# Optimization experiments

Hardware: AMD Instinct MI355X
Metric: run time of the kernel (lower is better)

## Reference

```python
import jax, jax.numpy as jnp
import numpy as np

B, F, E, K, O = 4096, 64, 16, 8, 32
NFEAT, HID = 100000, 1024
EPS = 1e-5
N_ITER = 50  # entmax bisection iterations (entmax package default)


def entmax15(x):
    # alpha=1.5 entmax via bisection, faithful to EntmaxBisectFunction.forward
    d = x.shape[-1]
    xs = x * 0.5  # X * (alpha - 1)
    mx = jnp.max(xs, axis=-1, keepdims=True)
    tau_lo = mx - 1.0                      # gp(1, 1.5) = 1
    tau_hi = mx - (1.0 / d) ** 0.5         # gp(1/d, 1.5)
    f_lo = jnp.sum(jnp.square(jnp.maximum(xs - tau_lo, 0.0)), -1, keepdims=True) - 1.0
    dm = tau_hi - tau_lo

    def body(i, carry):
        tau_lo, dm, _ = carry
        dm = dm * 0.5
        tau_m = tau_lo + dm
        f_m = jnp.sum(jnp.square(jnp.maximum(xs - tau_m, 0.0)), -1, keepdims=True) - 1.0
        tau_lo = jnp.where(f_m * f_lo >= 0, tau_m, tau_lo)
        return (tau_lo, dm, tau_m)

    _, _, tau_m = jax.lax.fori_loop(0, N_ITER, body, (tau_lo, dm, tau_lo))
    p = jnp.square(jnp.maximum(xs - tau_m, 0.0))
    return p / jnp.sum(p, -1, keepdims=True)


def bn_channels(x, g, b):
    # BatchNorm1d on (B, C, L): normalize over batch and L per channel C (train mode)
    m = jnp.mean(x, (0, 2), keepdims=True)
    v = jnp.var(x, (0, 2), keepdims=True)
    return (x - m) / jnp.sqrt(v + EPS) * g[None, :, None] + b[None, :, None]


def bn_feat(x, g, b):
    # BatchNorm1d on (B, C) (train mode, biased variance)
    m = jnp.mean(x, 0)
    v = jnp.var(x, 0)
    return (x - m) / jnp.sqrt(v + EPS) * g + b


def setup_inputs() -> dict:
    key = jax.random.key(0)
    ks = jax.random.split(key, 12)
    gain = 1.414
    aQ = gain * np.sqrt(6.0 / (O + E))
    aB = gain * np.sqrt(6.0 / (E + E))
    aV = gain * np.sqrt(6.0 / (O + F))
    D0 = K * O * E
    return {
        'x_id': jax.random.randint(ks[0], (B, F), 0, NFEAT),
        'x_value': jax.random.uniform(ks[1], (B, F), dtype=jnp.float32),
        'emb': jax.random.normal(ks[2], (NFEAT, E), dtype=jnp.float32) * 0.1,
        'emb_g': jnp.ones((F,), jnp.float32), 'emb_b': jnp.zeros((F,), jnp.float32),
        'Q': jax.random.uniform(ks[3], (K, O, E), jnp.float32, -aQ, aQ),
        'bil': jax.random.uniform(ks[4], (K, E, E), jnp.float32, -aB, aB),
        'vals': jax.random.uniform(ks[5], (K, O, F), jnp.float32, -aV, aV),
        'arm_g': jnp.ones((K * O,), jnp.float32), 'arm_b': jnp.zeros((K * O,), jnp.float32),
        'w1': jax.random.normal(ks[6], (HID, D0), jnp.float32) / np.sqrt(D0),
        'b1': jnp.zeros((HID,), jnp.float32),
        'g1': jnp.ones((HID,), jnp.float32), 'bt1': jnp.zeros((HID,), jnp.float32),
        'w2': jax.random.normal(ks[7], (HID, HID), jnp.float32) / np.sqrt(HID),
        'b2': jnp.zeros((HID,), jnp.float32),
        'g2': jnp.ones((HID,), jnp.float32), 'bt2': jnp.zeros((HID,), jnp.float32),
        'wout': jax.random.normal(ks[8], (1, HID), jnp.float32) / np.sqrt(HID),
        'bout': jnp.zeros((1,), jnp.float32),
    }


def reference(x_id, x_value, emb, emb_g, emb_b, Q, bil, vals, arm_g, arm_b,
              w1, b1, g1, bt1, w2, b2, g2, bt2, wout, bout):
    v = jnp.clip(x_value, 0.001, 1.0)
    xe = emb[x_id] * v[..., None]                       # B,F,E
    x_exp = bn_channels(jnp.exp(xe), emb_g, emb_b)       # B,F,E
    # bilinear attention scores + global context bias
    kq = jnp.einsum('kxy,koy->kox', bil, Q)              # K,O,E (fuse param contraction)
    sc = jnp.einsum('bfx,kox->bkof', xe, kq)             # B,K,O,F
    gc = jnp.einsum('bx,kox->bko', xe.sum(1), kq)        # B,K,O
    sg = entmax15(sc + gc[..., None])                    # B,K,O,F sparse gates
    aw = sg * vals[None]                                 # B,K,O,F
    arm = jnp.einsum('bfe,bkof->bkoe', x_exp, aw)        # B,K,O,E
    arm = arm.reshape(arm.shape[0], K * O, E)
    arm = bn_channels(arm, arm_g, arm_b).reshape(arm.shape[0], -1)
    h = jax.nn.relu(bn_feat(arm @ w1.T + b1, g1, bt1))
    h = jax.nn.relu(bn_feat(h @ w2.T + b2, g2, bt2))
    y = h @ wout.T + bout
    return y[:, 0]
```

## Files before the change

kernel.cpp:

```cpp
#include <hip/hip_runtime.h>

#define EPS 1e-5f

typedef __bf16 bf16;
typedef bf16 bf16x8 __attribute__((ext_vector_type(8)));
typedef float f32x4 __attribute__((ext_vector_type(4)));
typedef float f32x2 __attribute__((ext_vector_type(2)));

__device__ __forceinline__ void lds_cp16(void* lds, const void* g) {
  __builtin_amdgcn_global_load_lds(
      (const __attribute__((address_space(1))) void*)g,
      (__attribute__((address_space(3))) void*)lds, 16, 0, 0);
}

__device__ __forceinline__ f32x4 mfma_bf16(bf16x8 a, bf16x8 b, f32x4 c) {
  return __builtin_amdgcn_mfma_f32_16x16x32_bf16(a, b, c, 0, 0, 0);
}

__global__ void k_embed(const int* __restrict__ x_id, const float* __restrict__ x_val,
                        const float* __restrict__ emb, float* __restrict__ xe,
                        float* __restrict__ es_p, float* __restrict__ eq_p) {
  int t = threadIdx.x, bid = blockIdx.x;
  float s = 0.f, q = 0.f;
#pragma unroll
  for (int it = 0; it < 4; ++it) {
    int g = it * 65536 + bid * 256 + t;
    int id = x_id[g];
    float v = fminf(fmaxf(x_val[g], 0.001f), 1.0f);
    const float4* er = (const float4*)(emb + (size_t)id * 16);
    float4* xo = (float4*)(xe + (size_t)g * 16);
#pragma unroll
    for (int j = 0; j < 4; ++j) {
      float4 e = er[j];
      e.x *= v; e.y *= v; e.z *= v; e.w *= v;
      xo[j] = e;
      float a0 = __expf(e.x), a1 = __expf(e.y), a2 = __expf(e.z), a3 = __expf(e.w);
      s += (a0 + a1) + (a2 + a3);
      q += (a0 * a0 + a1 * a1) + (a2 * a2 + a3 * a3);
    }
  }
  __shared__ float rs[256], rq[256];
  rs[t] = s; rq[t] = q;
  __syncthreads();
  if (t < 64) {
    float S = rs[t] + rs[t + 64] + rs[t + 128] + rs[t + 192];
    float Q = rq[t] + rq[t + 64] + rq[t + 128] + rq[t + 192];
    es_p[bid * 64 + t] = S;
    eq_p[bid * 64 + t] = Q;
  }
}

__global__ void k_prep(const float* __restrict__ Qw, const float* __restrict__ bil,
                       float* __restrict__ kq, const float* __restrict__ es_p,
                       const float* __restrict__ eq_p, const float* __restrict__ g_,
                       const float* __restrict__ b_, float* __restrict__ oa,
                       float* __restrict__ ob) {
  int t = threadIdx.x;
  int k = t >> 5;
  float qv[16];
#pragma unroll
  for (int y = 0; y < 16; ++y) qv[y] = Qw[t * 16 + y];
  const float* bl = bil + k * 256;
#pragma unroll
  for (int x = 0; x < 16; ++x) {
    float s = 0.f;
#pragma unroll
    for (int y = 0; y < 16; ++y) s += bl[x * 16 + y] * qv[y];
    kq[t * 16 + x] = 0.5f * s;
  }
  if (t < 64) {
    float S = 0.f, Q = 0.f;
    for (int i = 0; i < 256; ++i) { S += es_p[i * 64 + t]; Q += eq_p[i * 64 + t]; }
    float mean = S * (1.0f / 65536.0f);
    float var = Q * (1.0f / 65536.0f) - mean * mean;
    float a = g_[t] * rsqrtf(var + EPS);
    oa[t] = a;
    ob[t] = b_[t] - mean * a;
  }
}

__global__ __launch_bounds__(256, 4) void k_attn(
    const float* __restrict__ xe_g, const float* __restrict__ kq_g,
    const float* __restrict__ eba, const float* __restrict__ ebb,
    const float* __restrict__ vals, bf16* __restrict__ arm) {
  __shared__ __align__(16) unsigned char smem[39168];
  float* s_xe = (float*)smem;
  float* s_sum = (float*)(smem + 4096);
  bf16* s_aw = (bf16*)smem;
  float* s_out = (float*)smem;
  bf16* s_X = (bf16*)(smem + 36864);
  const int t = threadIdx.x;
  const int b = blockIdx.x;
  const f32x2 z2 = {0.f, 0.f};

  ((float4*)s_xe)[t] = ((const float4*)(xe_g + (size_t)b * 1024))[t];
  __syncthreads();

  if (t < 16) {
    float s = 0.f;
#pragma unroll
    for (int f = 0; f < 64; ++f) s += s_xe[f * 16 + t];
    s_sum[t] = s;
  }
  {
    int f = t >> 2, e0 = (t & 3) * 4;
    float a = eba[f], c = ebb[f];
#pragma unroll
    for (int j = 0; j < 4; ++j) {
      float v = __expf(s_xe[f * 16 + e0 + j]) * a + c;
      s_X[(e0 + j) * 72 + f] = (bf16)v;
    }
  }
  __syncthreads();

  f32x2 kq2[8];
  {
    const f32x4* g4 = (const f32x4*)(kq_g + t * 16);
#pragma unroll
    for (int j = 0; j < 4; ++j) {
      f32x4 v = g4[j];
      kq2[2 * j] = __builtin_shufflevector(v, v, 0, 1);
      kq2[2 * j + 1] = __builtin_shufflevector(v, v, 2, 3);
    }
  }
  float gc;
  {
    const f32x2* ss = (const f32x2*)s_sum;
    f32x2 g2 = z2;
#pragma unroll
    for (int i = 0; i < 8; ++i) g2 += ss[i] * kq2[i];
    gc = g2.x + g2.y;
  }

  f32x2 xs2[32];
#pragma unroll
  for (int f = 0; f < 64; ++f) {
    const f32x4* xr = (const f32x4*)(s_xe + f * 16);
    f32x4 A0 = xr[0], A1 = xr[1], A2 = xr[2], A3 = xr[3];
    f32x2 acc = z2;
    acc += __builtin_shufflevector(A0, A0, 0, 1) * kq2[0];
    acc += __builtin_shufflevector(A0, A0, 2, 3) * kq2[1];
    acc += __builtin_shufflevector(A1, A1, 0, 1) * kq2[2];
    acc += __builtin_shufflevector(A1, A1, 2, 3) * kq2[3];
    acc += __builtin_shufflevector(A2, A2, 0, 1) * kq2[4];
    acc += __builtin_shufflevector(A2, A2, 2, 3) * kq2[5];
    acc += __builtin_shufflevector(A3, A3, 0, 1) * kq2[6];
    acc += __builtin_shufflevector(A3, A3, 2, 3) * kq2[7];
    float v = (acc.x + acc.y) + gc;
    if (f & 1) xs2[f >> 1].y = v; else xs2[f >> 1].x = v;
  }
  __syncthreads();

  f32x2 m2 = xs2[0];
#pragma unroll
  for (int i = 1; i < 32; ++i) m2 = __builtin_elementwise_max(m2, xs2[i]);
  float mx = fmaxf(m2.x, m2.y);

  float tau_lo = mx - 1.0f;
  float dm = 0.875f;
#pragma unroll
  for (int it = 0; it < 7; ++it) {
    dm *= 0.5f;
    float tm = tau_lo + dm;
    f32x2 t2 = {tm, tm};
    f32x2 c2 = z2;
#pragma unroll
    for (int i = 0; i < 32; ++i) {
      f32x2 d = xs2[i] - t2;
      d = __builtin_elementwise_max(d, z2);
      c2 += d * d;
    }
    tau_lo = ((c2.x + c2.y) - 1.0f >= 0.f) ? tm : tau_lo;
  }
  float tau = tau_lo + dm;
#pragma unroll
  for (int r = 0; r < 2; ++r) {
    f32x2 t2 = {tau, tau};
    f32x2 S2 = z2, Q2 = z2;
    float cnt = 0.f;
#pragma unroll
    for (int i = 0; i < 32; ++i) {
      f32x2 y = xs2[i] - t2;
      f32x2 m = __builtin_elementwise_max(y, z2);
      S2 += m; Q2 += m * m;
      cnt += (y.x > 0.f ? 1.f : 0.f) + (y.y > 0.f ? 1.f : 0.f);
    }
    float S1 = S2.x + S2.y, Q1 = Q2.x + Q2.y;
    float disc = fmaxf(S1 * S1 - cnt * (Q1 - 1.0f), 0.f);
    tau += (S1 - sqrtf(disc)) / cnt;
  }
  f32x2 Zv = z2;
  {
    f32x2 t2 = {tau, tau};
#pragma unroll
    for (int i = 0; i < 32; ++i) {
      f32x2 d = __builtin_elementwise_max(xs2[i] - t2, z2);
      f32x2 p = d * d;
      xs2[i] = p;
      Zv += p;
    }
  }
  float inv = 1.0f / (Zv.x + Zv.y);

  const float4* vg = (const float4*)(vals + t * 64);
#pragma unroll
  for (int f8 = 0; f8 < 64; f8 += 8) {
    float4 v0 = vg[f8 / 4], v1 = vg[f8 / 4 + 1];
    union { bf16 h[8]; uint4 u; } pk;
    pk.h[0] = (bf16)(xs2[f8 / 2].x * inv * v0.x);
    pk.h[1] = (bf16)(xs2[f8 / 2].y * inv * v0.y);
    pk.h[2] = (bf16)(xs2[f8 / 2 + 1].x * inv * v0.z);
    pk.h[3] = (bf16)(xs2[f8 / 2 + 1].y * inv * v0.w);
    pk.h[4] = (bf16)(xs2[f8 / 2 + 2].x * inv * v1.x);
    pk.h[5] = (bf16)(xs2[f8 / 2 + 2].y * inv * v1.y);
    pk.h[6] = (bf16)(xs2[f8 / 2 + 3].x * inv * v1.z);
    pk.h[7] = (bf16)(xs2[f8 / 2 + 3].y * inv * v1.w);
    *(uint4*)(s_aw + t * 72 + f8) = pk.u;
  }
  __syncthreads();

  const int w = t >> 6, lane = t & 63;
  f32x4 acc[4];
#pragma unroll
  for (int mt = 0; mt < 4; ++mt) acc[mt] = (f32x4){0.f, 0.f, 0.f, 0.f};
#pragma unroll
  for (int ks = 0; ks < 2; ++ks) {
    bf16x8 bfrag = *(const bf16x8*)(s_X + (lane & 15) * 72 + ks * 32 + (lane >> 4) * 8);
#pragma unroll
    for (int mt = 0; mt < 4; ++mt) {
      int row = (w * 4 + mt) * 16 + (lane & 15);
      bf16x8 afrag = *(const bf16x8*)(s_aw + row * 72 + ks * 32 + (lane >> 4) * 8);
      acc[mt] = mfma_bf16(afrag, bfrag, acc[mt]);
    }
  }
  __syncthreads();
#pragma unroll
  for (int mt = 0; mt < 4; ++mt) {
    int ko0 = (w * 4 + mt) * 16 + (lane >> 4) * 4;
#pragma unroll
    for (int r = 0; r < 4; ++r)
      s_out[(lane & 15) * 257 + ko0 + r] = acc[mt][r];
  }
  __syncthreads();
  union { bf16 h[16]; uint4 u[2]; } pk;
#pragma unroll
  for (int e = 0; e < 16; ++e) pk.h[e] = (bf16)s_out[e * 257 + t];
  uint4* dst = (uint4*)(arm + (size_t)b * 4096 + t * 16);
  dst[0] = pk.u[0];
  dst[1] = pk.u[1];
}

__global__ void k_armstats(const bf16* __restrict__ arm, float* __restrict__ as_p,
                           float* __restrict__ aq_p) {
  int t = threadIdx.x;
  int b0 = blockIdx.x * 64;
  float s = 0.f, q = 0.f;
  for (int i = 0; i < 64; ++i) {
    const bf16* p = arm + (size_t)(b0 + i) * 4096 + t * 16;
    bf16x8 v0 = *(const bf16x8*)p;
    bf16x8 v1 = *(const bf16x8*)(p + 8);
#pragma unroll
    for (int j = 0; j < 8; ++j) {
      float a = (float)v0[j], c = (float)v1[j];
      s += a + c; q += a * a + c * c;
    }
  }
  as_p[blockIdx.x * 256 + t] = s;
  aq_p[blockIdx.x * 256 + t] = q;
}

__global__ void k_cvtw(const float* __restrict__ w1, const float* __restrict__ w2,
                       const float* __restrict__ as_p, const float* __restrict__ aq_p,
                       const float* __restrict__ arm_g, bf16* __restrict__ d1,
                       bf16* __restrict__ d2) {
  int t = threadIdx.x, bid = blockIdx.x;
  if (bid < 256) {
    __shared__ float scale[256];
    float s = 0.f, q = 0.f;
    for (int i = 0; i < 64; ++i) { s += as_p[i * 256 + t]; q += aq_p[i * 256 + t]; }
    float mean = s * (1.0f / 65536.0f);
    float var = q * (1.0f / 65536.0f) - mean * mean;
    scale[t] = arm_g[t] * rsqrtf(var + EPS);
    __syncthreads();
#pragma unroll
    for (int it = 0; it < 16; ++it) {
      int i = it * 65536 + bid * 256 + t;
      float4 v = ((const float4*)w1)[i];
      float av = scale[(i >> 2) & 255];
      union { bf16 h[4]; uint2 u; } p;
      p.h[0] = (bf16)(v.x * av); p.h[1] = (bf16)(v.y * av);
      p.h[2] = (bf16)(v.z * av); p.h[3] = (bf16)(v.w * av);
      *(uint2*)(d1 + (size_t)i * 4) = p.u;
    }
  } else {
#pragma unroll
    for (int it = 0; it < 16; ++it) {
      int i = it * 16384 + (bid - 256) * 256 + t;
      float4 v = ((const float4*)w2)[i];
      union { bf16 h[4]; uint2 u; } p;
      p.h[0] = (bf16)v.x; p.h[1] = (bf16)v.y; p.h[2] = (bf16)v.z; p.h[3] = (bf16)v.w;
      *(uint2*)(d2 + (size_t)i * 4) = p.u;
    }
  }
}

__global__ __launch_bounds__(256, 2) void gemm_bt(
    const bf16* __restrict__ A, const bf16* __restrict__ Bw, float* __restrict__ C,
    float* __restrict__ sp, float* __restrict__ sq, int Kd) {
  __shared__ __align__(16) bf16 sA[128 * 32];
  __shared__ __align__(16) bf16 sB[64 * 32];
  __shared__ float sredS[4][64], sredQ[4][64];
  const int t = threadIdx.x;
  const int w = t >> 6, lane = t & 63;
  const int m0 = blockIdx.x * 128, n0 = blockIdx.y * 64;

  f32x4 acc[2][4];
#pragma unroll
  for (int i = 0; i < 2; ++i)
#pragma unroll
    for (int j = 0; j < 4; ++j) acc[i][j] = (f32x4){0.f, 0.f, 0.f, 0.f};

  for (int kt = 0; kt < Kd; kt += 32) {
#pragma unroll
    for (int c = 0; c < 2; ++c) {
      int idx = c * 256 + t;
      int row = idx >> 2, ch = idx & 3;
      int sch = ch ^ ((row >> 1) & 3);
      lds_cp16(sA + idx * 8, A + (size_t)(m0 + row) * Kd + kt + sch * 8);
    }
    {
      int row = t >> 2, ch = t & 3;
      int sch = ch ^ ((row >> 1) & 3);
      lds_cp16(sB + t * 8, Bw + (size_t)(n0 + row) * Kd + kt + sch * 8);
    }
    __syncthreads();
    bf16x8 af[2], bfr[4];
#pragma unroll
    for (int mt = 0; mt < 2; ++mt) {
      int row = w * 32 + mt * 16 + (lane & 15);
      int ch = (lane >> 4) ^ ((row >> 1) & 3);
      af[mt] = *(const bf16x8*)(sA + row * 32 + ch * 8);
    }
#pragma unroll
    for (int nt = 0; nt < 4; ++nt) {
      int row = nt * 16 + (lane & 15);
      int ch = (lane >> 4) ^ ((row >> 1) & 3);
      bfr[nt] = *(const bf16x8*)(sB + row * 32 + ch * 8);
    }
#pragma unroll
    for (int mt = 0; mt < 2; ++mt)
#pragma unroll
      for (int nt = 0; nt < 4; ++nt)
        acc[mt][nt] = mfma_bf16(af[mt], bfr[nt], acc[mt][nt]);
    __syncthreads();
  }

#pragma unroll
  for (int nt = 0; nt < 4; ++nt) {
    int ncol = n0 + nt * 16 + (lane & 15);
    float s = 0.f, q = 0.f;
#pragma unroll
    for (int mt = 0; mt < 2; ++mt) {
      int mr = m0 + w * 32 + mt * 16 + (lane >> 4) * 4;
#pragma unroll
      for (int r = 0; r < 4; ++r) {
        float v = acc[mt][nt][r];
        C[(size_t)(mr + r) * 1024 + ncol] = v;
        s += v; q += v * v;
      }
    }
    s += __shfl_xor(s, 16, 64); s += __shfl_xor(s, 32, 64);
    q += __shfl_xor(q, 16, 64); q += __shfl_xor(q, 32, 64);
    if (lane < 16) { sredS[w][nt * 16 + lane] = s; sredQ[w][nt * 16 + lane] = q; }
  }
  __syncthreads();
  if (t < 64) {
    float S = sredS[0][t] + sredS[1][t] + sredS[2][t] + sredS[3][t];
    float Q = sredQ[0][t] + sredQ[1][t] + sredQ[2][t] + sredQ[3][t];
    sp[blockIdx.x * 1024 + n0 + t] = S;
    sq[blockIdx.x * 1024 + n0 + t] = Q;
  }
}

__global__ void k_colfin(const float* __restrict__ sp, const float* __restrict__ sq,
                         const float* __restrict__ g_, const float* __restrict__ bt,
                         float* __restrict__ a, float* __restrict__ c) {
  int h = blockIdx.x * 256 + threadIdx.x;
  float S = 0.f, Q = 0.f;
  for (int i = 0; i < 32; ++i) { S += sp[i * 1024 + h]; Q += sq[i * 1024 + h]; }
  float mean = S * (1.0f / 4096.0f);
  float var = Q * (1.0f / 4096.0f) - mean * mean;
  float av = g_[h] * rsqrtf(var + EPS);
  a[h] = av;
  c[h] = bt[h] - mean * av;
}

__global__ void k_h1bf(const float* __restrict__ C1, const float* __restrict__ a,
                       const float* __restrict__ c, bf16* __restrict__ H1) {
  int i4 = blockIdx.x * 256 + threadIdx.x;
  int col0 = (i4 * 4) & 1023;
  float4 v = ((const float4*)C1)[i4];
  float4 av = *(const float4*)(a + col0);
  float4 cv = *(const float4*)(c + col0);
  union { bf16 h[4]; uint2 u; } pk;
  pk.h[0] = (bf16)fmaxf(v.x * av.x + cv.x, 0.f);
  pk.h[1] = (bf16)fmaxf(v.y * av.y + cv.y, 0.f);
  pk.h[2] = (bf16)fmaxf(v.z * av.z + cv.z, 0.f);
  pk.h[3] = (bf16)fmaxf(v.w * av.w + cv.w, 0.f);
  *(uint2*)(H1 + (size_t)i4 * 4) = pk.u;
}

__global__ __launch_bounds__(256) void k_out(const float* __restrict__ C2,
                                             const float* __restrict__ a,
                                             const float* __restrict__ c,
                                             const float* __restrict__ wout,
                                             const float* __restrict__ bout,
                                             float* __restrict__ y) {
  int t = threadIdx.x;
  int w = t >> 6, lane = t & 63;
  int row = blockIdx.x * 4 + w;
  const float* cr = C2 + (size_t)row * 1024;
  float s = 0.f;
#pragma unroll
  for (int j = 0; j < 16; ++j) {
    int col = j * 64 + lane;
    float v = fmaxf(cr[col] * a[col] + c[col], 0.f);
    s += v * wout[col];
  }
#pragma unroll
  for (int off = 32; off > 0; off >>= 1) s += __shfl_xor(s, off, 64);
  if (lane == 0) y[row] = s + bout[0];
}

extern "C" void kernel_launch(void* const* d_in, const int* in_sizes, int n_in,
                              void* d_out, int out_size, void* d_ws, size_t ws_size,
                              hipStream_t stream) {
  (void)in_sizes; (void)n_in; (void)out_size; (void)ws_size;
  const int* x_id = (const int*)d_in[0];
  const float* x_value = (const float*)d_in[1];
  const float* emb = (const float*)d_in[2];
  const float* emb_g = (const float*)d_in[3];
  const float* embb = (const float*)d_in[4];
  const float* Qw = (const float*)d_in[5];
  const float* bil = (const float*)d_in[6];
  const float* vals = (const float*)d_in[7];
  const float* arm_g = (const float*)d_in[8];
  const float* w1 = (const float*)d_in[10];
  const float* g1 = (const float*)d_in[12];
  const float* bt1 = (const float*)d_in[13];
  const float* w2 = (const float*)d_in[14];
  const float* g2 = (const float*)d_in[16];
  const float* bt2 = (const float*)d_in[17];
  const float* wout = (const float*)d_in[18];
  const float* bout = (const float*)d_in[19];

  char* w = (char*)d_ws;
  float* ws_A = (float*)w;
  bf16* ws_arm = (bf16*)(w + 16777216);
  bf16* ws_w1b = (bf16*)(w + 50331648);
  bf16* ws_H1 = ws_w1b;
  bf16* ws_w2b = (bf16*)(w + 58720256);
  float* ws_kq = (float*)(w + 60817408);
  float* misc = (float*)(w + 60833792);
  float* es_p = misc;
  float* eq_p = es_p + 16384;
  float* as_p = eq_p + 16384;
  float* aq_p = as_p + 16384;
  float* sp1 = aq_p + 16384;
  float* sq1 = sp1 + 32768;
  float* sp2 = sq1 + 32768;
  float* sq2 = sp2 + 32768;
  float* eb_a = sq2 + 32768;
  float* eb_b = eb_a + 64;
  float* a1c = eb_b + 64;
  float* c1c = a1c + 1024;
  float* a2c = c1c + 1024;
  float* c2c = a2c + 1024;

  k_embed<<<256, 256, 0, stream>>>(x_id, x_value, emb, ws_A, es_p, eq_p);
  k_prep<<<1, 256, 0, stream>>>(Qw, bil, ws_kq, es_p, eq_p, emb_g, embb, eb_a, eb_b);
  k_attn<<<4096, 256, 0, stream>>>(ws_A, ws_kq, eb_a, eb_b, vals, ws_arm);
  k_armstats<<<64, 256, 0, stream>>>(ws_arm, as_p, aq_p);
  k_cvtw<<<320, 256, 0, stream>>>(w1, w2, as_p, aq_p, arm_g, ws_w1b, ws_w2b);
  gemm_bt<<<dim3(32, 16), 256, 0, stream>>>(ws_arm, ws_w1b, ws_A, sp1, sq1, 4096);
  k_colfin<<<4, 256, 0, stream>>>(sp1, sq1, g1, bt1, a1c, c1c);
  k_h1bf<<<4096, 256, 0, stream>>>(ws_A, a1c, c1c, ws_H1);
  gemm_bt<<<dim3(32, 16), 256, 0, stream>>>(ws_H1, ws_w2b, ws_A, sp2, sq2, 1024);
  k_colfin<<<4, 256, 0, stream>>>(sp2, sq2, g2, bt2, a2c, c2c);
  k_out<<<1024, 256, 0, stream>>>(ws_A, a2c, c2c, wout, bout, (float*)d_out);
}
```

Baseline: 341.8 us.

## Split-K first MLP GEMM with 128x128 tiles and separate column-stats pass

```diff
diff --git a/kernel.cpp b/kernel.cpp
--- a/kernel.cpp
+++ b/kernel.cpp
@@ -79,7 +79,7 @@
   }
 }
 
-__global__ __launch_bounds__(256, 4) void k_attn(
+__global__ __launch_bounds__(256, 2) void k_attn(
     const float* __restrict__ xe_g, const float* __restrict__ kq_g,
     const float* __restrict__ eba, const float* __restrict__ ebb,
     const float* __restrict__ vals, bf16* __restrict__ arm) {
@@ -304,6 +304,85 @@
   }
 }
 
+__global__ __launch_bounds__(256, 2) void gemm_sk(
+    const bf16* __restrict__ A, const bf16* __restrict__ Bw,
+    float* __restrict__ P0, float* __restrict__ P1, int Ktot, int Kd) {
+  __shared__ __align__(16) bf16 sA[128 * 32];
+  __shared__ __align__(16) bf16 sB[128 * 32];
+  const int t = threadIdx.x;
+  const int w = t >> 6, lane = t & 63;
+  const int m0 = blockIdx.x * 128, n0 = blockIdx.y * 128;
+  const int k0 = blockIdx.z * Kd;
+  float* P = blockIdx.z ? P1 : P0;
+  const int wr = (w >> 1) * 64, wc = (w & 1) * 64;
+
+  f32x4 acc[4][4];
+#pragma unroll
+  for (int i = 0; i < 4; ++i)
+#pragma unroll
+    for (int j = 0; j < 4; ++j) acc[i][j] = (f32x4){0.f, 0.f, 0.f, 0.f};
+
+  for (int kt = 0; kt < Kd; kt += 32) {
+#pragma unroll
+    for (int c = 0; c < 2; ++c) {
+      int idx = c * 256 + t;
+      int row = idx >> 2, ch = idx & 3;
+      int sch = ch ^ ((row >> 1) & 3);
+      lds_cp16(sA + idx * 8, A + (size_t)(m0 + row) * Ktot + k0 + kt + sch * 8);
+      lds_cp16(sB + idx * 8, Bw + (size_t)(n0 + row) * Ktot + k0 + kt + sch * 8);
+    }
+    __syncthreads();
+    bf16x8 af[4], bfr[4];
+#pragma unroll
+    for (int mt = 0; mt < 4; ++mt) {
+      int row = wr + mt * 16 + (lane & 15);
+      int ch = (lane >> 4) ^ ((row >> 1) & 3);
+      af[mt] = *(const bf16x8*)(sA + row * 32 + ch * 8);
+    }
+#pragma unroll
+    for (int nt = 0; nt < 4; ++nt) {
+      int row = wc + nt * 16 + (lane & 15);
+      int ch = (lane >> 4) ^ ((row >> 1) & 3);
+      bfr[nt] = *(const bf16x8*)(sB + row * 32 + ch * 8);
+    }
+#pragma unroll
+    for (int mt = 0; mt < 4; ++mt)
+#pragma unroll
+      for (int nt = 0; nt < 4; ++nt)
+        acc[mt][nt] = mfma_bf16(af[mt], bfr[nt], acc[mt][nt]);
+    __syncthreads();
+  }
+
+#pragma unroll
+  for (int nt = 0; nt < 4; ++nt) {
+    int ncol = n0 + wc + nt * 16 + (lane & 15);
+#pragma unroll
+    for (int mt = 0; mt < 4; ++mt) {
+      int mr = m0 + wr + mt * 16 + (lane >> 4) * 4;
+#pragma unroll
+      for (int r = 0; r < 4; ++r)
+        P[(size_t)(mr + r) * 1024 + ncol] = acc[mt][nt][r];
+    }
+  }
+}
+
+__global__ void k_colstats(const float* __restrict__ P0, const float* __restrict__ P1,
+                           float* __restrict__ sp, float* __restrict__ sq) {
+  int t = threadIdx.x;
+  int r0 = blockIdx.x * 16;
+  float4 s4 = {0, 0, 0, 0}, q4 = {0, 0, 0, 0};
+  for (int i = 0; i < 16; ++i) {
+    float4 a = ((const float4*)(P0 + (size_t)(r0 + i) * 1024))[t];
+    float4 b = ((const float4*)(P1 + (size_t)(r0 + i) * 1024))[t];
+    float4 v;
+    v.x = a.x + b.x; v.y = a.y + b.y; v.z = a.z + b.z; v.w = a.w + b.w;
+    s4.x += v.x; s4.y += v.y; s4.z += v.z; s4.w += v.w;
+    q4.x += v.x * v.x; q4.y += v.y * v.y; q4.z += v.z * v.z; q4.w += v.w * v.w;
+  }
+  ((float4*)(sp + blockIdx.x * 1024))[t] = s4;
+  ((float4*)(sq + blockIdx.x * 1024))[t] = q4;
+}
+
 __global__ __launch_bounds__(256, 2) void gemm_bt(
     const bf16* __restrict__ A, const bf16* __restrict__ Bw, float* __restrict__ C,
     float* __restrict__ sp, float* __restrict__ sq, int Kd) {
@@ -384,10 +463,10 @@
 
 __global__ void k_colfin(const float* __restrict__ sp, const float* __restrict__ sq,
                          const float* __restrict__ g_, const float* __restrict__ bt,
-                         float* __restrict__ a, float* __restrict__ c) {
+                         float* __restrict__ a, float* __restrict__ c, int npart) {
   int h = blockIdx.x * 256 + threadIdx.x;
   float S = 0.f, Q = 0.f;
-  for (int i = 0; i < 32; ++i) { S += sp[i * 1024 + h]; Q += sq[i * 1024 + h]; }
+  for (int i = 0; i < npart; ++i) { S += sp[i * 1024 + h]; Q += sq[i * 1024 + h]; }
   float mean = S * (1.0f / 4096.0f);
   float var = Q * (1.0f / 4096.0f) - mean * mean;
   float av = g_[h] * rsqrtf(var + EPS);
@@ -395,18 +474,20 @@
   c[h] = bt[h] - mean * av;
 }
 
-__global__ void k_h1bf(const float* __restrict__ C1, const float* __restrict__ a,
-                       const float* __restrict__ c, bf16* __restrict__ H1) {
+__global__ void k_h1bf(const float* __restrict__ P0, const float* __restrict__ P1,
+                       const float* __restrict__ a, const float* __restrict__ c,
+                       bf16* __restrict__ H1) {
   int i4 = blockIdx.x * 256 + threadIdx.x;
   int col0 = (i4 * 4) & 1023;
-  float4 v = ((const float4*)C1)[i4];
+  float4 u = ((const float4*)P0)[i4];
+  float4 v = ((const float4*)P1)[i4];
   float4 av = *(const float4*)(a + col0);
   float4 cv = *(const float4*)(c + col0);
   union { bf16 h[4]; uint2 u; } pk;
-  pk.h[0] = (bf16)fmaxf(v.x * av.x + cv.x, 0.f);
-  pk.h[1] = (bf16)fmaxf(v.y * av.y + cv.y, 0.f);
-  pk.h[2] = (bf16)fmaxf(v.z * av.z + cv.z, 0.f);
-  pk.h[3] = (bf16)fmaxf(v.w * av.w + cv.w, 0.f);
+  pk.h[0] = (bf16)fmaxf((u.x + v.x) * av.x + cv.x, 0.f);
+  pk.h[1] = (bf16)fmaxf((u.y + v.y) * av.y + cv.y, 0.f);
+  pk.h[2] = (bf16)fmaxf((u.z + v.z) * av.z + cv.z, 0.f);
+  pk.h[3] = (bf16)fmaxf((u.w + v.w) * av.w + cv.w, 0.f);
   *(uint2*)(H1 + (size_t)i4 * 4) = pk.u;
 }
 
@@ -457,18 +538,19 @@
   char* w = (char*)d_ws;
   float* ws_A = (float*)w;
   bf16* ws_arm = (bf16*)(w + 16777216);
-  bf16* ws_w1b = (bf16*)(w + 50331648);
+  float* ws_D = (float*)(w + 50331648);
+  bf16* ws_w1b = (bf16*)(w + 67108864);
   bf16* ws_H1 = ws_w1b;
-  bf16* ws_w2b = (bf16*)(w + 58720256);
-  float* ws_kq = (float*)(w + 60817408);
-  float* misc = (float*)(w + 60833792);
+  bf16* ws_w2b = (bf16*)(w + 75497472);
+  float* ws_kq = (float*)(w + 77594624);
+  float* misc = (float*)(w + 77611008);
   float* es_p = misc;
   float* eq_p = es_p + 16384;
   float* as_p = eq_p + 16384;
   float* aq_p = as_p + 16384;
   float* sp1 = aq_p + 16384;
-  float* sq1 = sp1 + 32768;
-  float* sp2 = sq1 + 32768;
+  float* sq1 = sp1 + 262144;
+  float* sp2 = sq1 + 262144;
   float* sq2 = sp2 + 32768;
   float* eb_a = sq2 + 32768;
   float* eb_b = eb_a + 64;
@@ -482,10 +564,11 @@
   k_attn<<<4096, 256, 0, stream>>>(ws_A, ws_kq, eb_a, eb_b, vals, ws_arm);
   k_armstats<<<64, 256, 0, stream>>>(ws_arm, as_p, aq_p);
   k_cvtw<<<320, 256, 0, stream>>>(w1, w2, as_p, aq_p, arm_g, ws_w1b, ws_w2b);
-  gemm_bt<<<dim3(32, 16), 256, 0, stream>>>(ws_arm, ws_w1b, ws_A, sp1, sq1, 4096);
-  k_colfin<<<4, 256, 0, stream>>>(sp1, sq1, g1, bt1, a1c, c1c);
-  k_h1bf<<<4096, 256, 0, stream>>>(ws_A, a1c, c1c, ws_H1);
+  gemm_sk<<<dim3(32, 8, 2), 256, 0, stream>>>(ws_arm, ws_w1b, ws_A, ws_D, 4096, 2048);
+  k_colstats<<<256, 256, 0, stream>>>(ws_A, ws_D, sp1, sq1);
+  k_colfin<<<4, 256, 0, stream>>>(sp1, sq1, g1, bt1, a1c, c1c, 256);
+  k_h1bf<<<4096, 256, 0, stream>>>(ws_A, ws_D, a1c, c1c, ws_H1);
   gemm_bt<<<dim3(32, 16), 256, 0, stream>>>(ws_H1, ws_w2b, ws_A, sp2, sq2, 1024);
-  k_colfin<<<4, 256, 0, stream>>>(sp2, sq2, g2, bt2, a2c, c2c);
+  k_colfin<<<4, 256, 0, stream>>>(sp2, sq2, g2, bt2, a2c, c2c, 32);
   k_out<<<1024, 256, 0, stream>>>(ws_A, a2c, c2c, wout, bout, (float*)d_out);
 }
```

Result: slower. 410.5 us (+20.1%).

## Compute attention scores with split-bf16 MFMA and wave-distributed entmax

Applied to the files above, without the earlier changes.

```diff
diff --git a/kernel.cpp b/kernel.cpp
--- a/kernel.cpp
+++ b/kernel.cpp
@@ -5,7 +5,6 @@
 typedef __bf16 bf16;
 typedef bf16 bf16x8 __attribute__((ext_vector_type(8)));
 typedef float f32x4 __attribute__((ext_vector_type(4)));
-typedef float f32x2 __attribute__((ext_vector_type(2)));
 
 __device__ __forceinline__ void lds_cp16(void* lds, const void* g) {
   __builtin_amdgcn_global_load_lds(
@@ -51,10 +50,10 @@
 }
 
 __global__ void k_prep(const float* __restrict__ Qw, const float* __restrict__ bil,
-                       float* __restrict__ kq, const float* __restrict__ es_p,
-                       const float* __restrict__ eq_p, const float* __restrict__ g_,
-                       const float* __restrict__ b_, float* __restrict__ oa,
-                       float* __restrict__ ob) {
+                       bf16* __restrict__ kqh, bf16* __restrict__ kql,
+                       const float* __restrict__ es_p, const float* __restrict__ eq_p,
+                       const float* __restrict__ g_, const float* __restrict__ b_,
+                       float* __restrict__ oa, float* __restrict__ ob) {
   int t = threadIdx.x;
   int k = t >> 5;
   float qv[16];
@@ -66,7 +65,10 @@
     float s = 0.f;
 #pragma unroll
     for (int y = 0; y < 16; ++y) s += bl[x * 16 + y] * qv[y];
-    kq[t * 16 + x] = 0.5f * s;
+    s *= 0.5f;
+    bf16 h = (bf16)s;
+    kqh[t * 16 + x] = h;
+    kql[t * 16 + x] = (bf16)(s - (float)h);
   }
   if (t < 64) {
     float S = 0.f, Q = 0.f;
@@ -79,19 +81,23 @@
   }
 }
 
-__global__ __launch_bounds__(256, 4) void k_attn(
-    const float* __restrict__ xe_g, const float* __restrict__ kq_g,
-    const float* __restrict__ eba, const float* __restrict__ ebb,
-    const float* __restrict__ vals, bf16* __restrict__ arm) {
-  __shared__ __align__(16) unsigned char smem[39168];
+__global__ __launch_bounds__(256, 3) void k_attn(
+    const float* __restrict__ xe_g, const bf16* __restrict__ kqh_g,
+    const bf16* __restrict__ kql_g, const float* __restrict__ eba,
+    const float* __restrict__ ebb, const float* __restrict__ vals,
+    bf16* __restrict__ arm) {
+  __shared__ __align__(16) unsigned char smem[47424];
+  bf16* s_aw = (bf16*)smem;
   float* s_xe = (float*)smem;
-  float* s_sum = (float*)(smem + 4096);
-  bf16* s_aw = (bf16*)smem;
-  float* s_out = (float*)smem;
   bf16* s_X = (bf16*)(smem + 36864);
+  bf16* s_Ah = (bf16*)(smem + 39168);
+  bf16* s_Al = (bf16*)(smem + 43264);
+  float* s_sum = (float*)(smem + 47360);
   const int t = threadIdx.x;
   const int b = blockIdx.x;
-  const f32x2 z2 = {0.f, 0.f};
+  const int w = t >> 6, lane = t & 63;
+  const int q = lane >> 4, ln = lane & 15;
+  const f32x4 z4 = {0.f, 0.f, 0.f, 0.f};
 
   ((float4*)s_xe)[t] = ((const float4*)(xe_g + (size_t)b * 1024))[t];
   __syncthreads();
@@ -113,141 +119,147 @@
   }
   __syncthreads();
 
-  f32x2 kq2[8];
   {
-    const f32x4* g4 = (const f32x4*)(kq_g + t * 16);
+    int f = t >> 2, x0 = (t & 3) * 4;
+    union { bf16 h[4]; unsigned long long u; } ph, pl, pz;
+    pz.u = 0ull;
 #pragma unroll
     for (int j = 0; j < 4; ++j) {
-      f32x4 v = g4[j];
-      kq2[2 * j] = __builtin_shufflevector(v, v, 0, 1);
-      kq2[2 * j + 1] = __builtin_shufflevector(v, v, 2, 3);
-    }
-  }
-  float gc;
-  {
-    const f32x2* ss = (const f32x2*)s_sum;
-    f32x2 g2 = z2;
-#pragma unroll
-    for (int i = 0; i < 8; ++i) g2 += ss[i] * kq2[i];
-    gc = g2.x + g2.y;
-  }
-
-  f32x2 xs2[32];
-#pragma unroll
-  for (int f = 0; f < 64; ++f) {
-    const f32x4* xr = (const f32x4*)(s_xe + f * 16);
-    f32x4 A0 = xr[0], A1 = xr[1], A2 = xr[2], A3 = xr[3];
-    f32x2 acc = z2;
-    acc += __builtin_shufflevector(A0, A0, 0, 1) * kq2[0];
-    acc += __builtin_shufflevector(A0, A0, 2, 3) * kq2[1];
-    acc += __builtin_shufflevector(A1, A1, 0, 1) * kq2[2];
-    acc += __builtin_shufflevector(A1, A1, 2, 3) * kq2[3];
-    acc += __builtin_shufflevector(A2, A2, 0, 1) * kq2[4];
-    acc += __builtin_shufflevector(A2, A2, 2, 3) * kq2[5];
-    acc += __builtin_shufflevector(A3, A3, 0, 1) * kq2[6];
-    acc += __builtin_shufflevector(A3, A3, 2, 3) * kq2[7];
-    float v = (acc.x + acc.y) + gc;
-    if (f & 1) xs2[f >> 1].y = v; else xs2[f >> 1].x = v;
+      float v = s_xe[f * 16 + x0 + j] + s_sum[x0 + j];
+      bf16 h = (bf16)v;
+      ph.h[j] = h;
+      pl.h[j] = (bf16)(v - (float)h);
+    }
+    *(unsigned long long*)(s_Ah + f * 32 + x0) = ph.u;
+    *(unsigned long long*)(s_Al + f * 32 + x0) = pl.u;
+    *(unsigned long long*)(s_Ah + f * 32 + 16 + x0) = pz.u;
+    *(unsigned long long*)(s_Al + f * 32 + 16 + x0) = pz.u;
   }
   __syncthreads();
 
-  f32x2 m2 = xs2[0];
-#pragma unroll
-  for (int i = 1; i < 32; ++i) m2 = __builtin_elementwise_max(m2, xs2[i]);
-  float mx = fmaxf(m2.x, m2.y);
-
-  float tau_lo = mx - 1.0f;
-  float dm = 0.875f;
-#pragma unroll
-  for (int it = 0; it < 7; ++it) {
-    dm *= 0.5f;
-    float tm = tau_lo + dm;
-    f32x2 t2 = {tm, tm};
-    f32x2 c2 = z2;
-#pragma unroll
-    for (int i = 0; i < 32; ++i) {
-      f32x2 d = xs2[i] - t2;
-      d = __builtin_elementwise_max(d, z2);
-      c2 += d * d;
-    }
-    tau_lo = ((c2.x + c2.y) - 1.0f >= 0.f) ? tm : tau_lo;
-  }
-  float tau = tau_lo + dm;
-#pragma unroll
-  for (int r = 0; r < 2; ++r) {
-    f32x2 t2 = {tau, tau};
-    f32x2 S2 = z2, Q2 = z2;
-    float cnt = 0.f;
-#pragma unroll
-    for (int i = 0; i < 32; ++i) {
-      f32x2 y = xs2[i] - t2;
-      f32x2 m = __builtin_elementwise_max(y, z2);
-      S2 += m; Q2 += m * m;
-      cnt += (y.x > 0.f ? 1.f : 0.f) + (y.y > 0.f ? 1.f : 0.f);
-    }
-    float S1 = S2.x + S2.y, Q1 = Q2.x + Q2.y;
-    float disc = fmaxf(S1 * S1 - cnt * (Q1 - 1.0f), 0.f);
-    tau += (S1 - sqrtf(disc)) / cnt;
-  }
-  f32x2 Zv = z2;
-  {
-    f32x2 t2 = {tau, tau};
-#pragma unroll
-    for (int i = 0; i < 32; ++i) {
-      f32x2 d = __builtin_elementwise_max(xs2[i] - t2, z2);
-      f32x2 p = d * d;
-      xs2[i] = p;
-      Zv += p;
-    }
-  }
-  float inv = 1.0f / (Zv.x + Zv.y);
-
-  const float4* vg = (const float4*)(vals + t * 64);
-#pragma unroll
-  for (int f8 = 0; f8 < 64; f8 += 8) {
-    float4 v0 = vg[f8 / 4], v1 = vg[f8 / 4 + 1];
-    union { bf16 h[8]; uint4 u; } pk;
-    pk.h[0] = (bf16)(xs2[f8 / 2].x * inv * v0.x);
-    pk.h[1] = (bf16)(xs2[f8 / 2].y * inv * v0.y);
-    pk.h[2] = (bf16)(xs2[f8 / 2 + 1].x * inv * v0.z);
-    pk.h[3] = (bf16)(xs2[f8 / 2 + 1].y * inv * v0.w);
-    pk.h[4] = (bf16)(xs2[f8 / 2 + 2].x * inv * v1.x);
-    pk.h[5] = (bf16)(xs2[f8 / 2 + 2].y * inv * v1.y);
-    pk.h[6] = (bf16)(xs2[f8 / 2 + 3].x * inv * v1.z);
-    pk.h[7] = (bf16)(xs2[f8 / 2 + 3].y * inv * v1.w);
-    *(uint4*)(s_aw + t * 72 + f8) = pk.u;
+  bf16x8 Ah[4], Al[4];
+#pragma unroll
+  for (int ft = 0; ft < 4; ++ft) {
+    int row = ft * 16 + ln;
+    Ah[ft] = *(const bf16x8*)(s_Ah + row * 32 + q * 8);
+    Al[ft] = *(const bf16x8*)(s_Al + row * 32 + q * 8);
+  }
+
+#pragma unroll
+  for (int gi = 0; gi < 4; ++gi) {
+    const int ko = (w * 4 + gi) * 16 + ln;
+    bf16x8 Bh, Bl;
+#pragma unroll
+    for (int j = 0; j < 8; ++j) { Bh[j] = (bf16)0.f; Bl[j] = (bf16)0.f; }
+    if (q < 2) {
+      Bh = *(const bf16x8*)(kqh_g + ko * 16 + q * 8);
+      Bl = *(const bf16x8*)(kql_g + ko * 16 + q * 8);
+    }
+    f32x4 xs[4];
+#pragma unroll
+    for (int ft = 0; ft < 4; ++ft) {
+      f32x4 a = z4;
+      a = mfma_bf16(Ah[ft], Bh, a);
+      a = mfma_bf16(Al[ft], Bh, a);
+      a = mfma_bf16(Ah[ft], Bl, a);
+      xs[ft] = a;
+    }
+
+    f32x4 mm = __builtin_elementwise_max(__builtin_elementwise_max(xs[0], xs[1]),
+                                         __builtin_elementwise_max(xs[2], xs[3]));
+    float mx = fmaxf(fmaxf(mm.x, mm.y), fmaxf(mm.z, mm.w));
+    mx = fmaxf(mx, __shfl_xor(mx, 16, 64));
+    mx = fmaxf(mx, __shfl_xor(mx, 32, 64));
+
+    float tau_lo = mx - 1.0f;
+    float dm = 0.875f;
+#pragma unroll
+    for (int it = 0; it < 7; ++it) {
+      dm *= 0.5f;
+      float tm = tau_lo + dm;
+      f32x4 t4 = {tm, tm, tm, tm};
+      f32x4 c4 = z4;
+#pragma unroll
+      for (int ft = 0; ft < 4; ++ft) {
+        f32x4 d = __builtin_elementwise_max(xs[ft] - t4, z4);
+        c4 += d * d;
+      }
+      float s = (c4.x + c4.y) + (c4.z + c4.w);
+      s += __shfl_xor(s, 16, 64);
+      s += __shfl_xor(s, 32, 64);
+      tau_lo = (s - 1.0f >= 0.f) ? tm : tau_lo;
+    }
+    float tau = tau_lo + dm;
+#pragma unroll
+    for (int r = 0; r < 2; ++r) {
+      f32x4 t4 = {tau, tau, tau, tau};
+      f32x4 S4 = z4, Q4 = z4;
+      float cnt = 0.f;
+#pragma unroll
+      for (int ft = 0; ft < 4; ++ft) {
+        f32x4 y = xs[ft] - t4;
+        f32x4 m = __builtin_elementwise_max(y, z4);
+        S4 += m; Q4 += m * m;
+        cnt += (y.x > 0.f ? 1.f : 0.f) + (y.y > 0.f ? 1.f : 0.f) +
+               (y.z > 0.f ? 1.f : 0.f) + (y.w > 0.f ? 1.f : 0.f);
+      }
+      float S1 = (S4.x + S4.y) + (S4.z + S4.w);
+      float Q1 = (Q4.x + Q4.y) + (Q4.z + Q4.w);
+      S1 += __shfl_xor(S1, 16, 64); S1 += __shfl_xor(S1, 32, 64);
+      Q1 += __shfl_xor(Q1, 16, 64); Q1 += __shfl_xor(Q1, 32, 64);
+      cnt += __shfl_xor(cnt, 16, 64); cnt += __shfl_xor(cnt, 32, 64);
+      float disc = fmaxf(S1 * S1 - cnt * (Q1 - 1.0f), 0.f);
+      tau += (S1 - sqrtf(disc)) / cnt;
+    }
+    f32x4 t4 = {tau, tau, tau, tau};
+    f32x4 Z4 = z4;
+#pragma unroll
+    for (int ft = 0; ft < 4; ++ft) {
+      f32x4 d = __builtin_elementwise_max(xs[ft] - t4, z4);
+      f32x4 p = d * d;
+      xs[ft] = p;
+      Z4 += p;
+    }
+    float Z = (Z4.x + Z4.y) + (Z4.z + Z4.w);
+    Z += __shfl_xor(Z, 16, 64);
+    Z += __shfl_xor(Z, 32, 64);
+    float inv = 1.0f / Z;
+
+#pragma unroll
+    for (int ft = 0; ft < 4; ++ft) {
+      int f0 = ft * 16 + q * 4;
+      float4 vv = *(const float4*)(vals + ko * 64 + f0);
+      union { bf16 h[4]; unsigned long long u; } pk;
+      pk.h[0] = (bf16)(xs[ft].x * inv * vv.x);
+      pk.h[1] = (bf16)(xs[ft].y * inv * vv.y);
+      pk.h[2] = (bf16)(xs[ft].z * inv * vv.z);
+      pk.h[3] = (bf16)(xs[ft].w * inv * vv.w);
+      *(unsigned long long*)(s_aw + ko * 72 + f0) = pk.u;
+    }
   }
   __syncthreads();
 
-  const int w = t >> 6, lane = t & 63;
   f32x4 acc[4];
 #pragma unroll
-  for (int mt = 0; mt < 4; ++mt) acc[mt] = (f32x4){0.f, 0.f, 0.f, 0.f};
+  for (int mt = 0; mt < 4; ++mt) acc[mt] = z4;
 #pragma unroll
   for (int ks = 0; ks < 2; ++ks) {
-    bf16x8 bfrag = *(const bf16x8*)(s_X + (lane & 15) * 72 + ks * 32 + (lane >> 4) * 8);
+    bf16x8 bfrag = *(const bf16x8*)(s_X + ln * 72 + ks * 32 + q * 8);
 #pragma unroll
     for (int mt = 0; mt < 4; ++mt) {
-      int row = (w * 4 + mt) * 16 + (lane & 15);
-      bf16x8 afrag = *(const bf16x8*)(s_aw + row * 72 + ks * 32 + (lane >> 4) * 8);
+      int row = (w * 4 + mt) * 16 + ln;
+      bf16x8 afrag = *(const bf16x8*)(s_aw + row * 72 + ks * 32 + q * 8);
       acc[mt] = mfma_bf16(afrag, bfrag, acc[mt]);
     }
   }
-  __syncthreads();
+  bf16* armb = arm + (size_t)b * 4096;
 #pragma unroll
   for (int mt = 0; mt < 4; ++mt) {
-    int ko0 = (w * 4 + mt) * 16 + (lane >> 4) * 4;
+    int ko0 = (w * 4 + mt) * 16 + q * 4;
 #pragma unroll
     for (int r = 0; r < 4; ++r)
-      s_out[(lane & 15) * 257 + ko0 + r] = acc[mt][r];
-  }
-  __syncthreads();
-  union { bf16 h[16]; uint4 u[2]; } pk;
-#pragma unroll
-  for (int e = 0; e < 16; ++e) pk.h[e] = (bf16)s_out[e * 257 + t];
-  uint4* dst = (uint4*)(arm + (size_t)b * 4096 + t * 16);
-  dst[0] = pk.u[0];
-  dst[1] = pk.u[1];
+      armb[(ko0 + r) * 16 + ln] = (bf16)acc[mt][r];
+  }
 }
 
 __global__ void k_armstats(const bf16* __restrict__ arm, float* __restrict__ as_p,
@@ -460,7 +472,8 @@
   bf16* ws_w1b = (bf16*)(w + 50331648);
   bf16* ws_H1 = ws_w1b;
   bf16* ws_w2b = (bf16*)(w + 58720256);
-  float* ws_kq = (float*)(w + 60817408);
+  bf16* ws_kqh = (bf16*)(w + 60817408);
+  bf16* ws_kql = (bf16*)(w + 60825600);
   float* misc = (float*)(w + 60833792);
   float* es_p = misc;
   float* eq_p = es_p + 16384;
@@ -478,8 +491,9 @@
   float* c2c = a2c + 1024;
 
   k_embed<<<256, 256, 0, stream>>>(x_id, x_value, emb, ws_A, es_p, eq_p);
-  k_prep<<<1, 256, 0, stream>>>(Qw, bil, ws_kq, es_p, eq_p, emb_g, embb, eb_a, eb_b);
-  k_attn<<<4096, 256, 0, stream>>>(ws_A, ws_kq, eb_a, eb_b, vals, ws_arm);
+  k_prep<<<1, 256, 0, stream>>>(Qw, bil, ws_kqh, ws_kql, es_p, eq_p, emb_g, embb,
+                                eb_a, eb_b);
+  k_attn<<<4096, 256, 0, stream>>>(ws_A, ws_kqh, ws_kql, eb_a, eb_b, vals, ws_arm);
   k_armstats<<<64, 256, 0, stream>>>(ws_arm, as_p, aq_p);
   k_cvtw<<<320, 256, 0, stream>>>(w1, w2, as_p, aq_p, arm_g, ws_w1b, ws_w2b);
   gemm_bt<<<dim3(32, 16), 256, 0, stream>>>(ws_arm, ws_w1b, ws_A, sp1, sq1, 4096);
```

Result: no change. 339.6 us (-0.6%).
